# Performance work log

Hardware: AMD Instinct MI355X
Metric: run time of the kernel (lower is better)

## Reference

```python
import jax, jax.numpy as jnp
import numpy as np
from jax import lax

EPS = 1e-5
PATCH = 4

def _ln(x, g, b):
    m = jnp.mean(x, -1, keepdims=True)
    v = jnp.mean(jnp.square(x - m), -1, keepdims=True)
    return (x - m) * lax.rsqrt(v + EPS) * g + b

def _gelu(x):
    return jax.nn.gelu(x, approximate=False)  # torch nn.GELU default (erf)

def setup_inputs() -> dict:
    key = jax.random.key(0)
    B, D, H, M, L, C = 8, 256, 16, 1024, 24, 1000
    S = (32 // PATCH) ** 2 + 1  # 65 tokens
    ks = iter(jax.random.split(key, 16))
    def w(shape, fan_in):
        return jax.random.normal(next(ks), shape, jnp.float32) * (fan_in ** -0.5)
    z = lambda *s: jnp.zeros(s, jnp.float32)
    o = lambda *s: jnp.ones(s, jnp.float32)
    return {
        'x': jax.random.normal(next(ks), (B, 3, 32, 32), jnp.float32),
        'conv_w': w((D, 3, PATCH, PATCH), 3 * PATCH * PATCH),
        'conv_b': z(D),
        'cls_tok': jax.random.normal(next(ks), (1, 1, D), jnp.float32),
        'pos_emb': jax.random.normal(next(ks), (1, S, D), jnp.float32),
        'Wqkv': w((L, H, D, 3 * D), D),   # per-layer, per-head full-D qkv
        'bqkv': z(L, H, 3 * D),
        'Wo': w((L, H * D, D), H * D),
        'bo': z(L, D),
        'ln1_g': o(L, D), 'ln1_b': z(L, D),
        'ln2_g': o(L, D), 'ln2_b': z(L, D),
        'Wm1': w((L, D, M), D), 'bm1': z(L, M),
        'Wm2': w((L, M, D), M), 'bm2': z(L, D),
        'Wh1': w((D, M), D), 'bh1': z(M),
        'Wh2': w((M, D), M), 'bh2': z(D),
        'Wh3': w((D, C), D), 'bh3': z(C),
    }

def reference(x, conv_w, conv_b, cls_tok, pos_emb, Wqkv, bqkv, Wo, bo,
              ln1_g, ln1_b, ln2_g, ln2_b, Wm1, bm1, Wm2, bm2,
              Wh1, bh1, Wh2, bh2, Wh3, bh3):
    B = x.shape[0]
    D = conv_w.shape[0]
    H = Wqkv.shape[1]
    scale = (D / H) ** -0.5  # quirk: full-D attention scaled by head_dim
    # patch embed: conv stride=kernel=PATCH, then flatten HW -> tokens
    y = lax.conv_general_dilated(x, conv_w, (PATCH, PATCH), 'VALID',
                                 dimension_numbers=('NCHW', 'OIHW', 'NCHW'))
    y = y + conv_b[None, :, None, None]
    y = y.reshape(B, D, -1).transpose(0, 2, 1)  # [B, N, D]
    y = jnp.concatenate([jnp.broadcast_to(cls_tok, (B, 1, D)), y], axis=1) + pos_emb
    S = y.shape[1]

    def layer(carry, p):
        Wq, bq, Wo_, bo_, g1, b1_, g2, b2_, W1, bm1_, W2, bm2_ = p
        z = _ln(carry, g1, b1_)
        qkv = jnp.einsum('bsd,hde->bhse', z, Wq) + bq[None, :, None, :]  # [B,H,S,3D]
        q, k, v = jnp.split(qkv, 3, axis=-1)
        attn = jax.nn.softmax(jnp.einsum('bhsd,bhtd->bhst', q, k) * scale, axis=-1)
        o = jnp.einsum('bhst,bhtd->bhsd', attn, v)
        o = o.transpose(0, 2, 1, 3).reshape(B, S, -1)  # concat heads -> [B,S,H*D]
        y1 = o @ Wo_ + bo_ + carry
        z2 = _ln(y1, g2, b2_)
        h = _gelu(_gelu(z2 @ W1 + bm1_) @ W2 + bm2_)  # GELU after BOTH linears
        return h + y1, None

    y, _ = lax.scan(layer, y, (Wqkv, bqkv, Wo, bo, ln1_g, ln1_b, ln2_g, ln2_b,
                               Wm1, bm1, Wm2, bm2))
    cls = y[:, 0, :]
    h = _gelu(cls @ Wh1 + bh1)
    h = _gelu(h @ Wh2 + bh2)
    return h @ Wh3 + bh3
```

## Files before the change

### kernel.cpp

```cpp
#include <hip/hip_runtime.h>
#include <hip/hip_bf16.h>

typedef __attribute__((ext_vector_type(8))) short short8;
typedef __attribute__((ext_vector_type(4))) float f32x4;

__device__ __forceinline__ float gelu_f(float x) {
  return 0.5f * x * (1.0f + erff(x * 0.70710678118654752440f));
}
__device__ __forceinline__ short f2bf(float f) {
  unsigned u = __float_as_uint(f);
  u += 0x7fffu + ((u >> 16) & 1u);
  return (short)(u >> 16);
}
__device__ __forceinline__ float bf2f(short s) {
  return __uint_as_float(((unsigned)(unsigned short)s) << 16);
}
__device__ __forceinline__ void split2(float v, short& h, short& l) {
  h = f2bf(v);
  l = f2bf(v - bf2f(h));
}
__device__ __forceinline__ int swz(int col, int row) {
  return (col & ~63) | ((col & 63) ^ ((row & 7) << 3));
}

__device__ __forceinline__ float block_sum_256(float v, float* sb) {
#pragma unroll
  for (int o = 1; o < 64; o <<= 1) v += __shfl_xor(v, o, 64);
  if ((threadIdx.x & 63) == 0) sb[threadIdx.x >> 6] = v;
  __syncthreads();
  float r = sb[0] + sb[1] + sb[2] + sb[3];
  __syncthreads();
  return r;
}

struct PrepArgs {
  const float *x, *cw, *cb, *cls, *pos, *ln1g, *ln1b;
  float* tok;
  short *zh, *zl;
  const float *Wqkv, *Wo, *Wm1, *Wm2;
  short *Wqh, *Wql, *Woh, *Wol, *W1h, *W1l, *W2h, *W2l;
};

__device__ void conv_body(const float* __restrict__ in,
                          short* __restrict__ outh, short* __restrict__ outl,
                          int K, int ldn, int group, long long gstride, int bx,
                          int by, float* tile ) {
  const int n0 = bx * 128;
  const int k0 = by * 64;
  const int tid = threadIdx.x;
  {
    const int j = tid & 31;
    const int kb = tid >> 5;
    const int n = n0 + 4 * j;
    const long long nbase = (long long)(n / group) * gstride + (n % group);
#pragma unroll
    for (int i = 0; i < 8; ++i) {
      const int k = kb * 8 + i;
      float4 v4 = *(const float4*)(in + nbase + (long long)(k0 + k) * ldn);
      tile[0 * 2112 + k * 33 + j] = v4.x;
      tile[1 * 2112 + k * 33 + j] = v4.y;
      tile[2 * 2112 + k * 33 + j] = v4.z;
      tile[3 * 2112 + k * 33 + j] = v4.w;
    }
  }
  __syncthreads();
  {
    const int r = tid >> 1;
    const int hf = tid & 1;
    const int n = n0 + r;
    const int e = r & 3, jj = r >> 2;
    const int g8 = n & 7;
    const float* te = tile + e * 2112 + jj;
    const long long obase = (long long)n * K + k0;
#pragma unroll
    for (int j2 = 0; j2 < 4; ++j2) {
      const int s = hf * 4 + j2;
      const int m = s ^ g8;
      short8 sh, sl;
#pragma unroll
      for (int e8 = 0; e8 < 8; ++e8) {
        float v = te[(m * 8 + e8) * 33];
        short h, L;
        split2(v, h, L);
        sh[e8] = h;
        sl[e8] = L;
      }
      *(short8*)(outh + obase + s * 8) = sh;
      *(short8*)(outl + obase + s * 8) = sl;
    }
  }
}

__global__ __launch_bounds__(256) void prep_kernel(PrepArgs p) {
  __shared__ __align__(16) float smem[4 * 64 * 33];
  const int t = blockIdx.x;
  if (t < 520) {
    float* sb = smem;
    int r = t;
    int b = r / 65, s = r % 65;
    int d = threadIdx.x;
    float val;
    if (s == 0) {
      val = p.cls[d];
    } else {
      int pp = s - 1, pi = pp >> 3, pj = pp & 7;
      const float* xb = p.x + b * 3072 + pi * 4 * 32 + pj * 4;
      const float* w = p.cw + d * 48;
      float acc = p.cb[d];
#pragma unroll
      for (int c = 0; c < 3; ++c)
#pragma unroll
        for (int i = 0; i < 4; ++i)
#pragma unroll
          for (int j = 0; j < 4; ++j)
            acc += xb[c * 1024 + i * 32 + j] * w[c * 16 + i * 4 + j];
      val = acc;
    }
    val += p.pos[s * 256 + d];
    p.tok[r * 256 + d] = val;
    float mean = block_sum_256(val, sb) * (1.0f / 256.0f);
    float dv = val - mean;
    float var = block_sum_256(dv * dv, sb) * (1.0f / 256.0f);
    float z = dv * rsqrtf(var + 1e-5f) * p.ln1g[d] + p.ln1b[d];
    short h, L;
    split2(z, h, L);
    p.zh[r * 256 + swz(d, r)] = h;
    p.zl[r * 256 + swz(d, r)] = L;
    return;
  }
  const int u = t - 520;
  const int layer = u / 576;
  const int r = u % 576;
  if (r < 384) {
    conv_body(p.Wqkv + (long long)layer * 3145728,
              p.Wqh + (long long)layer * 3145728,
              p.Wql + (long long)layer * 3145728, 256, 768, 768, 196608LL,
              r % 96, r / 96, smem);
  } else if (r < 512) {
    int v = r - 384;
    conv_body(p.Wo + (long long)layer * 1048576,
              p.Woh + (long long)layer * 1048576,
              p.Wol + (long long)layer * 1048576, 4096, 256, 1 << 30, 0LL,
              v % 2, v / 2, smem);
  } else if (r < 544) {
    int v = r - 512;
    conv_body(p.Wm1 + (long long)layer * 262144,
              p.W1h + (long long)layer * 262144,
              p.W1l + (long long)layer * 262144, 256, 1024, 1 << 30, 0LL,
              v % 8, v / 8, smem);
  } else {
    int v = r - 544;
    conv_body(p.Wm2 + (long long)layer * 262144,
              p.W2h + (long long)layer * 262144,
              p.W2l + (long long)layer * 262144, 1024, 256, 1 << 30, 0LL,
              v % 2, v / 2, smem);
  }
}

__global__ __launch_bounds__(256) void gemm_x3(
    const short* __restrict__ Ah, const short* __restrict__ Al,
    const short* __restrict__ Bh, const short* __restrict__ Bl, int M, int N,
    int K, int kchunk, const float* __restrict__ bias,
    float* __restrict__ out32, float* __restrict__ P) {
  __shared__ short Ash[128 * 64];
  __shared__ short Asl[128 * 64];
  __shared__ short Bsh[128 * 64];
  __shared__ short Bsl[128 * 64];
  const int tid = threadIdx.x;
  const int w = tid >> 6, l = tid & 63;
  const int col0 = blockIdx.x * 128;
  const int row0 = blockIdx.y * 128;
  const int kbeg = blockIdx.z * kchunk;
  const int kend = kbeg + kchunk;
  const int wm = w >> 1, wn = w & 1;

  f32x4 acc[4][4];
#pragma unroll
  for (int i = 0; i < 4; ++i)
#pragma unroll
    for (int j = 0; j < 4; ++j) acc[i][j] = (f32x4)(0.f);

  const int srow = l >> 3;
  const int sslot = l & 7;

#define STAGE4(dst, src, rbase)                                            \
  {                                                                        \
    _Pragma("unroll") for (int i = 0; i < 4; ++i) {                        \
      int r = (w * 4 + i) * 8 + srow;                                      \
      const char* gp =                                                     \
          (const char*)(src + (size_t)(rbase + r) * K + k0) + sslot * 16;  \
      short* lp = dst + (w * 4 + i) * 512;                                 \
      __builtin_amdgcn_global_load_lds(                                    \
          (const __attribute__((address_space(1))) unsigned int*)gp,       \
          (__attribute__((address_space(3))) unsigned int*)lp, 16, 0, 0);  \
    }                                                                      \
  }

  for (int k0 = kbeg; k0 < kend; k0 += 64) {
    __syncthreads();
    STAGE4(Ash, Ah, row0)
    STAGE4(Asl, Al, row0)
    STAGE4(Bsh, Bh, col0)
    STAGE4(Bsl, Bl, col0)
    __syncthreads();
#pragma unroll
    for (int kc = 0; kc < 2; ++kc) {
      short8 ah[4], al[4], bh[4], bl[4];
#pragma unroll
      for (int mi = 0; mi < 4; ++mi) {
        int row = wm * 64 + mi * 16 + (l & 15);
        int slot = (kc * 4 + (l >> 4)) ^ (row & 7);
        ah[mi] = *(const short8*)&Ash[row * 64 + slot * 8];
        al[mi] = *(const short8*)&Asl[row * 64 + slot * 8];
      }
#pragma unroll
      for (int ni = 0; ni < 4; ++ni) {
        int row = wn * 64 + ni * 16 + (l & 15);
        int slot = (kc * 4 + (l >> 4)) ^ (row & 7);
        bh[ni] = *(const short8*)&Bsh[row * 64 + slot * 8];
        bl[ni] = *(const short8*)&Bsl[row * 64 + slot * 8];
      }
#pragma unroll
      for (int mi = 0; mi < 4; ++mi)
#pragma unroll
        for (int ni = 0; ni < 4; ++ni) {
          acc[mi][ni] = __builtin_amdgcn_mfma_f32_16x16x32_bf16(
              ah[mi], bh[ni], acc[mi][ni], 0, 0, 0);
          acc[mi][ni] = __builtin_amdgcn_mfma_f32_16x16x32_bf16(
              ah[mi], bl[ni], acc[mi][ni], 0, 0, 0);
          acc[mi][ni] = __builtin_amdgcn_mfma_f32_16x16x32_bf16(
              al[mi], bh[ni], acc[mi][ni], 0, 0, 0);
        }
    }
  }
#undef STAGE4

#pragma unroll
  for (int mi = 0; mi < 4; ++mi) {
#pragma unroll
    for (int ni = 0; ni < 4; ++ni) {
      int row = row0 + wm * 64 + mi * 16 + (l >> 4) * 4;
      int col = col0 + wn * 64 + ni * 16 + (l & 15);
      if (out32) {
        float bc = bias ? bias[col] : 0.f;
#pragma unroll
        for (int r = 0; r < 4; ++r)
          if (row + r < M)
            out32[(size_t)(row + r) * N + col] = acc[mi][ni][r] + bc;
      } else {
        float* Pz = P + (size_t)blockIdx.z * M * N;
#pragma unroll
        for (int r = 0; r < 4; ++r)
          if (row + r < M) Pz[(size_t)(row + r) * N + col] = acc[mi][ni][r];
      }
    }
  }
}

template <int NSPLIT>
__global__ __launch_bounds__(256) void epilogue_kernel(
    const float* __restrict__ P, int M, int N, const float* __restrict__ bias,
    const float* __restrict__ res, float* __restrict__ out32,
    short* __restrict__ o16h, short* __restrict__ o16l, int act,
    const float* __restrict__ g, const float* __restrict__ bln,
    short* __restrict__ z16h, short* __restrict__ z16l) {
  __shared__ float sb[4];
  int r = blockIdx.x;
  float myval = 0.f;
  for (int c = threadIdx.x; c < N; c += 256) {
    const float* pp = P + (long long)r * N + c;
    float acc = 0.f;
#pragma unroll
    for (int s = 0; s < NSPLIT; ++s) acc += pp[(long long)s * M * N];
    acc += bias[c];
    if (act) acc = gelu_f(acc);
    if (res) acc += res[(long long)r * N + c];
    if (out32) out32[(long long)r * N + c] = acc;
    if (o16h) {
      short h, L;
      split2(acc, h, L);
      o16h[(long long)r * N + swz(c, r)] = h;
      o16l[(long long)r * N + swz(c, r)] = L;
    }
    myval = acc;
  }
  if (z16h) {
    float mean = block_sum_256(myval, sb) * (1.f / 256.f);
    float dv = myval - mean;
    float var = block_sum_256(dv * dv, sb) * (1.f / 256.f);
    float z = dv * rsqrtf(var + 1e-5f) * g[threadIdx.x] + bln[threadIdx.x];
    short h, L;
    split2(z, h, L);
    z16h[r * 256 + swz((int)threadIdx.x, r)] = h;
    z16l[r * 256 + swz((int)threadIdx.x, r)] = L;
  }
}

#define AROWS 17
__global__ __launch_bounds__(256) void attn_kernel(const float* __restrict__ qkv,
                                                   short* __restrict__ Oh,
                                                   short* __restrict__ Ol) {
  __shared__ float qs[AROWS + 1][256];
  __shared__ float Ks[68][68];
  __shared__ float ps[AROWS][66];
  __shared__ float mx[20], sm[20];
  const int tid = threadIdx.x;
  const int s0 = blockIdx.x * AROWS;
  const int bh = blockIdx.y;
  const int b = bh >> 4, h = bh & 15;
  const long long base = (long long)(b * 65) * 12288 + h * 768;

#pragma unroll
  for (int i = 0; i < AROWS; ++i) {
    int s = s0 + i;
    qs[i][tid] = (s < 65) ? qkv[base + (long long)s * 12288 + tid] : 0.f;
  }

  const int up = tid / 17, tg = tid % 17;
  const int i0 = up * 2, t0 = tg * 4;
  const bool uval = (tid < 153);
  float acc[2][4] = {};
  for (int dc = 0; dc < 256; dc += 64) {
    __syncthreads();
    for (int idx = tid; idx < 65 * 64; idx += 256) {
      int t = idx >> 6, dd = idx & 63;
      Ks[t][dd] = qkv[base + (long long)t * 12288 + 256 + dc + dd];
    }
    __syncthreads();
    if (uval) {
#pragma unroll
      for (int d4 = 0; d4 < 64; d4 += 4) {
        float4 qa = *(const float4*)&qs[i0][dc + d4];
        float4 qb = *(const float4*)&qs[i0 + 1][dc + d4];
#pragma unroll
        for (int c = 0; c < 4; ++c) {
          float4 kv = *(const float4*)&Ks[t0 + c][d4];
          acc[0][c] += qa.x * kv.x + qa.y * kv.y + qa.z * kv.z + qa.w * kv.w;
          acc[1][c] += qb.x * kv.x + qb.y * kv.y + qb.z * kv.z + qb.w * kv.w;
        }
      }
    }
  }
  if (uval) {
#pragma unroll
    for (int ii = 0; ii < 2; ++ii) {
      int i = i0 + ii;
      if (i < AROWS && (s0 + i) < 65) {
#pragma unroll
        for (int c = 0; c < 4; ++c) {
          int t = t0 + c;
          if (t < 65) ps[i][t] = acc[ii][c] * 0.25f;
        }
      }
    }
  }
  __syncthreads();

  if (tid < 68) {
    int row = tid >> 2, j = tid & 3;
    float m = -1e30f;
    if ((s0 + row) < 65)
      for (int t = j; t < 65; t += 4) m = fmaxf(m, ps[row][t]);
    m = fmaxf(m, __shfl_xor(m, 1, 64));
    m = fmaxf(m, __shfl_xor(m, 2, 64));
    if (j == 0) mx[row] = m;
  }
  __syncthreads();
  for (int idx = tid; idx < AROWS * 65; idx += 256) {
    int r = idx / 65, t = idx % 65;
    if ((s0 + r) < 65) ps[r][t] = expf(ps[r][t] - mx[r]);
  }
  __syncthreads();
  if (tid < 68) {
    int row = tid >> 2, j = tid & 3;
    float s = 0.f;
    if ((s0 + row) < 65)
      for (int t = j; t < 65; t += 4) s += ps[row][t];
    s += __shfl_xor(s, 1, 64);
    s += __shfl_xor(s, 2, 64);
    if (j == 0) sm[row] = 1.f / s;
  }
  __syncthreads();
  for (int idx = tid; idx < AROWS * 65; idx += 256) {
    int r = idx / 65, t = idx % 65;
    if ((s0 + r) < 65) ps[r][t] *= sm[r];
  }
  __syncthreads();

  float oacc[AROWS];
#pragma unroll
  for (int i = 0; i < AROWS; ++i) oacc[i] = 0.f;
  const float* vp = qkv + base + 512 + tid;
  for (int t = 0; t < 65; ++t) {
    float vtd = vp[(long long)t * 12288];
#pragma unroll
    for (int i = 0; i < AROWS; ++i) oacc[i] += ps[i][t] * vtd;
  }
#pragma unroll
  for (int i = 0; i < AROWS; ++i) {
    int s = s0 + i;
    if (s < 65) {
      int row = b * 65 + s;
      int col = h * 256 + ((tid & ~63) | ((tid & 63) ^ ((row & 7) << 3)));
      short hh, LL;
      split2(oacc[i], hh, LL);
      Oh[(long long)row * 4096 + col] = hh;
      Ol[(long long)row * 4096 + col] = LL;
    }
  }
}

template <int KS>
__global__ __launch_bounds__(256) void head_gemm2(
    const float* __restrict__ A, int lda, const float* __restrict__ B,
    const float* __restrict__ bias, float* __restrict__ C, int N, int K,
    int act) {
  constexpr int COLS = 256 / KS;
  __shared__ float red[KS][COLS];
  const int lane = threadIdx.x % COLS;
  const int ks = threadIdx.x / COLS;
  const int c = blockIdx.x * COLS + lane;
  const int r = blockIdx.y;
  const float* a = A + (long long)r * lda;
  float acc = 0.f;
  const int kc = K / KS;
  if (c < N) {
    const float* ap = a + ks * kc;
    const float* bp = B + (long long)(ks * kc) * N + c;
#pragma unroll 8
    for (int k = 0; k < kc; ++k) acc += ap[k] * bp[(long long)k * N];
  }
  red[ks][lane] = acc;
  __syncthreads();
  if (ks == 0 && c < N) {
    float v = bias[c];
#pragma unroll
    for (int s = 0; s < KS; ++s) v += red[s][lane];
    if (act) v = gelu_f(v);
    C[(long long)r * N + c] = v;
  }
}

extern "C" void kernel_launch(void* const* d_in, const int* in_sizes, int n_in,
                              void* d_out, int out_size, void* d_ws,
                              size_t ws_size, hipStream_t stream) {
  const float* x = (const float*)d_in[0];
  const float* conv_w = (const float*)d_in[1];
  const float* conv_b = (const float*)d_in[2];
  const float* cls = (const float*)d_in[3];
  const float* pos = (const float*)d_in[4];
  const float* Wqkv = (const float*)d_in[5];
  const float* bqkv = (const float*)d_in[6];
  const float* Wo = (const float*)d_in[7];
  const float* bo = (const float*)d_in[8];
  const float* ln1g = (const float*)d_in[9];
  const float* ln1b = (const float*)d_in[10];
  const float* ln2g = (const float*)d_in[11];
  const float* ln2b = (const float*)d_in[12];
  const float* Wm1 = (const float*)d_in[13];
  const float* bm1 = (const float*)d_in[14];
  const float* Wm2 = (const float*)d_in[15];
  const float* bm2 = (const float*)d_in[16];
  const float* Wh1 = (const float*)d_in[17];
  const float* bh1 = (const float*)d_in[18];
  const float* Wh2 = (const float*)d_in[19];
  const float* bh2 = (const float*)d_in[20];
  const float* Wh3 = (const float*)d_in[21];
  const float* bh3 = (const float*)d_in[22];
  float* out = (float*)d_out;

  float* ws = (float*)d_ws;
  float* tok = ws;
  float* y1 = ws + 163840;
  float* Pb = ws + 327680;
  float* qkvf = ws + 2457600;
  short* zh = (short*)(ws + 8847360);
  short* zl = (short*)(ws + 8929280);
  short* Oh = (short*)(ws + 9011200);
  short* Ol = (short*)(ws + 10321920);
  short* h1h = (short*)(ws + 11632640);
  short* h1l = (short*)(ws + 11960320);
  float* hh1 = ws + 12288000;
  float* hh2 = ws + 12296192;
  short* Wqh = (short*)(ws + 12298240);
  short* Wql = (short*)(ws + 50046976);
  short* Woh = (short*)(ws + 87795712);
  short* Wol_ = (short*)(ws + 100378624);
  short* W1h = (short*)(ws + 112961536);
  short* W1l = (short*)(ws + 116107264);
  short* W2h = (short*)(ws + 119252992);
  short* W2l = (short*)(ws + 122398720);

  const int M = 520;

  PrepArgs p;
  p.x = x; p.cw = conv_w; p.cb = conv_b; p.cls = cls; p.pos = pos;
  p.ln1g = ln1g; p.ln1b = ln1b;
  p.tok = tok; p.zh = zh; p.zl = zl;
  p.Wqkv = Wqkv; p.Wo = Wo; p.Wm1 = Wm1; p.Wm2 = Wm2;
  p.Wqh = Wqh; p.Wql = Wql; p.Woh = Woh; p.Wol = Wol_;
  p.W1h = W1h; p.W1l = W1l; p.W2h = W2h; p.W2l = W2l;
  prep_kernel<<<520 + 24 * 576, 256, 0, stream>>>(p);

  for (int l = 0; l < 24; ++l) {
    const short* Wqhl = Wqh + (long long)l * 3145728;
    const short* Wqll = Wql + (long long)l * 3145728;
    const short* Wohl = Woh + (long long)l * 1048576;
    const short* Woll = Wol_ + (long long)l * 1048576;
    const short* W1hl = W1h + (long long)l * 262144;
    const short* W1ll = W1l + (long long)l * 262144;
    const short* W2hl = W2h + (long long)l * 262144;
    const short* W2ll = W2l + (long long)l * 262144;
    const float* bq = bqkv + l * 12288;
    const float* bol = bo + l * 256;
    const float* b1 = bm1 + l * 1024;
    const float* b2 = bm2 + l * 256;

    gemm_x3<<<dim3(96, 5, 1), 256, 0, stream>>>(zh, zl, Wqhl, Wqll, M, 12288,
                                                256, 256, bq, qkvf, nullptr);

    attn_kernel<<<dim3(4, 128), 256, 0, stream>>>(qkvf, Oh, Ol);

    gemm_x3<<<dim3(2, 5, 16), 256, 0, stream>>>(Oh, Ol, Wohl, Woll, M, 256,
                                                4096, 256, nullptr, nullptr,
                                                Pb);
    epilogue_kernel<16><<<520, 256, 0, stream>>>(
        Pb, M, 256, bol, tok, y1, nullptr, nullptr, 0, ln2g + l * 256,
        ln2b + l * 256, zh, zl);

    gemm_x3<<<dim3(8, 5, 4), 256, 0, stream>>>(zh, zl, W1hl, W1ll, M, 1024,
                                               256, 64, nullptr, nullptr, Pb);
    epilogue_kernel<4><<<520, 256, 0, stream>>>(Pb, M, 1024, b1, nullptr,
                                                nullptr, h1h, h1l, 1, nullptr,
                                                nullptr, nullptr, nullptr);

    gemm_x3<<<dim3(2, 5, 16), 256, 0, stream>>>(h1h, h1l, W2hl, W2ll, M, 256,
                                                1024, 64, nullptr, nullptr,
                                                Pb);
    const float* ng = (l < 23) ? ln1g + (l + 1) * 256 : nullptr;
    const float* nb = (l < 23) ? ln1b + (l + 1) * 256 : nullptr;
    short* nzh = (l < 23) ? zh : nullptr;
    short* nzl = (l < 23) ? zl : nullptr;
    epilogue_kernel<16><<<520, 256, 0, stream>>>(Pb, M, 256, b2, y1, tok,
                                                 nullptr, nullptr, 1, ng, nb,
                                                 nzh, nzl);
  }

  head_gemm2<4><<<dim3(16, 8), 256, 0, stream>>>(tok, 16640, Wh1, bh1, hh1,
                                                 1024, 256, 1);
  head_gemm2<8><<<dim3(8, 8), 256, 0, stream>>>(hh1, 1024, Wh2, bh2, hh2, 256,
                                                1024, 1);
  head_gemm2<4><<<dim3(16, 8), 256, 0, stream>>>(hh2, 256, Wh3, bh3, out, 1000,
                                                 256, 0);
}
```

Baseline: 3.092 ms.

## Fuse output projection into attention kernel with fp32 per-head partials

The attention kernel now multiplies its per-head output by that head's 256x256 slice of Wo in fp32 and writes per-head partial sums into the buffer the epilogue already reduces over 16 splits. This removes the separate split-bf16 x3 Wo GEMM, the bf16 hi/lo writes of the attention output, and the Wo conversion in the prep kernel. In exchange, each attention block streams a 256 KB Wo slice with scalar FMAs, and the four row-blocks of each (b,h) re-read the same slice.

```diff
diff --git a/kernel.cpp b/kernel.cpp
--- a/kernel.cpp
+++ b/kernel.cpp
@@ -37,8 +37,8 @@
   const float *x, *cw, *cb, *cls, *pos, *ln1g, *ln1b;
   float* tok;
   short *zh, *zl;
-  const float *Wqkv, *Wo, *Wm1, *Wm2;
-  short *Wqh, *Wql, *Woh, *Wol, *W1h, *W1l, *W2h, *W2l;
+  const float *Wqkv, *Wm1, *Wm2;
+  short *Wqh, *Wql, *W1h, *W1l, *W2h, *W2l;
 };
 
 __device__ void conv_body(const float* __restrict__ in,
@@ -129,27 +129,21 @@
     return;
   }
   const int u = t - 520;
-  const int layer = u / 576;
-  const int r = u % 576;
+  const int layer = u / 448;
+  const int r = u % 448;
   if (r < 384) {
     conv_body(p.Wqkv + (long long)layer * 3145728,
               p.Wqh + (long long)layer * 3145728,
               p.Wql + (long long)layer * 3145728, 256, 768, 768, 196608LL,
               r % 96, r / 96, smem);
-  } else if (r < 512) {
+  } else if (r < 416) {
     int v = r - 384;
-    conv_body(p.Wo + (long long)layer * 1048576,
-              p.Woh + (long long)layer * 1048576,
-              p.Wol + (long long)layer * 1048576, 4096, 256, 1 << 30, 0LL,
-              v % 2, v / 2, smem);
-  } else if (r < 544) {
-    int v = r - 512;
     conv_body(p.Wm1 + (long long)layer * 262144,
               p.W1h + (long long)layer * 262144,
               p.W1l + (long long)layer * 262144, 256, 1024, 1 << 30, 0LL,
               v % 8, v / 8, smem);
   } else {
-    int v = r - 544;
+    int v = r - 416;
     conv_body(p.Wm2 + (long long)layer * 262144,
               p.W2h + (long long)layer * 262144,
               p.W2l + (long long)layer * 262144, 1024, 256, 1 << 30, 0LL,
@@ -297,9 +291,9 @@
 }
 
 #define AROWS 17
-__global__ __launch_bounds__(256) void attn_kernel(const float* __restrict__ qkv,
-                                                   short* __restrict__ Oh,
-                                                   short* __restrict__ Ol) {
+__global__ __launch_bounds__(256) void attn_wo_kernel(
+    const float* __restrict__ qkv, const float* __restrict__ Wol,
+    float* __restrict__ Pb) {
   __shared__ float qs[AROWS + 1][256];
   __shared__ float Ks[68][68];
   __shared__ float ps[AROWS][66];
@@ -396,17 +390,27 @@
 #pragma unroll
     for (int i = 0; i < AROWS; ++i) oacc[i] += ps[i][t] * vtd;
   }
+
+  __syncthreads();
+#pragma unroll
+  for (int i = 0; i < AROWS; ++i) qs[i][tid] = oacc[i];
+  __syncthreads();
+
+  const float* Wslice = Wol + (long long)h * 256 * 256;
+  float pacc[AROWS];
+#pragma unroll
+  for (int i = 0; i < AROWS; ++i) pacc[i] = 0.f;
+#pragma unroll 4
+  for (int d = 0; d < 256; ++d) {
+    float wv = Wslice[d * 256 + tid];
+#pragma unroll
+    for (int i = 0; i < AROWS; ++i) pacc[i] += qs[i][d] * wv;
+  }
+  float* Ph = Pb + (size_t)h * 520 * 256;
 #pragma unroll
   for (int i = 0; i < AROWS; ++i) {
     int s = s0 + i;
-    if (s < 65) {
-      int row = b * 65 + s;
-      int col = h * 256 + ((tid & ~63) | ((tid & 63) ^ ((row & 7) << 3)));
-      short hh, LL;
-      split2(oacc[i], hh, LL);
-      Oh[(long long)row * 4096 + col] = hh;
-      Ol[(long long)row * 4096 + col] = LL;
-    }
+    if (s < 65) Ph[(size_t)(b * 65 + s) * 256 + tid] = pacc[i];
   }
 }
 
@@ -476,16 +480,12 @@
   float* qkvf = ws + 2457600;
   short* zh = (short*)(ws + 8847360);
   short* zl = (short*)(ws + 8929280);
-  short* Oh = (short*)(ws + 9011200);
-  short* Ol = (short*)(ws + 10321920);
   short* h1h = (short*)(ws + 11632640);
   short* h1l = (short*)(ws + 11960320);
   float* hh1 = ws + 12288000;
   float* hh2 = ws + 12296192;
   short* Wqh = (short*)(ws + 12298240);
   short* Wql = (short*)(ws + 50046976);
-  short* Woh = (short*)(ws + 87795712);
-  short* Wol_ = (short*)(ws + 100378624);
   short* W1h = (short*)(ws + 112961536);
   short* W1l = (short*)(ws + 116107264);
   short* W2h = (short*)(ws + 119252992);
@@ -497,16 +497,14 @@
   p.x = x; p.cw = conv_w; p.cb = conv_b; p.cls = cls; p.pos = pos;
   p.ln1g = ln1g; p.ln1b = ln1b;
   p.tok = tok; p.zh = zh; p.zl = zl;
-  p.Wqkv = Wqkv; p.Wo = Wo; p.Wm1 = Wm1; p.Wm2 = Wm2;
-  p.Wqh = Wqh; p.Wql = Wql; p.Woh = Woh; p.Wol = Wol_;
+  p.Wqkv = Wqkv; p.Wm1 = Wm1; p.Wm2 = Wm2;
+  p.Wqh = Wqh; p.Wql = Wql;
   p.W1h = W1h; p.W1l = W1l; p.W2h = W2h; p.W2l = W2l;
-  prep_kernel<<<520 + 24 * 576, 256, 0, stream>>>(p);
+  prep_kernel<<<520 + 24 * 448, 256, 0, stream>>>(p);
 
   for (int l = 0; l < 24; ++l) {
     const short* Wqhl = Wqh + (long long)l * 3145728;
     const short* Wqll = Wql + (long long)l * 3145728;
-    const short* Wohl = Woh + (long long)l * 1048576;
-    const short* Woll = Wol_ + (long long)l * 1048576;
     const short* W1hl = W1h + (long long)l * 262144;
     const short* W1ll = W1l + (long long)l * 262144;
     const short* W2hl = W2h + (long long)l * 262144;
@@ -519,11 +517,9 @@
     gemm_x3<<<dim3(96, 5, 1), 256, 0, stream>>>(zh, zl, Wqhl, Wqll, M, 12288,
                                                 256, 256, bq, qkvf, nullptr);
 
-    attn_kernel<<<dim3(4, 128), 256, 0, stream>>>(qkvf, Oh, Ol);
-
-    gemm_x3<<<dim3(2, 5, 16), 256, 0, stream>>>(Oh, Ol, Wohl, Woll, M, 256,
-                                                4096, 256, nullptr, nullptr,
-                                                Pb);
+    attn_wo_kernel<<<dim3(4, 128), 256, 0, stream>>>(
+        qkvf, Wo + (long long)l * 1048576, Pb);
+
     epilogue_kernel<16><<<520, 256, 0, stream>>>(
         Pb, M, 256, bol, tok, y1, nullptr, nullptr, 0, ln2g + l * 256,
         ln2b + l * 256, zh, zl);
```

Result: slower. 3.302 ms (+6.8%).
